# Kernel tuning notes

Hardware: AMD Instinct MI355X
Metric: run time of the kernel (lower is better)

## Reference

```python
import jax, jax.numpy as jnp
import numpy as np

B, F, C, H, W = 4, 16, 768, 16, 16   # video: b f c h w
L, M = 64, 16                        # audio: b c l m
NH = 12                              # num_heads
WS_V = 4                             # local_window (video window size, frames)
GROUPS = 32                          # GroupNorm32
EPS = 1e-5


def group_norm(x, scale, bias):
    # x: [b, c, t]; normalize over (channels-within-group, t)
    b, c, t = x.shape
    xg = x.reshape(b, GROUPS, c // GROUPS, t)
    mu = xg.mean(axis=(2, 3), keepdims=True)
    var = xg.var(axis=(2, 3), keepdims=True)
    xg = (xg - mu) * jax.lax.rsqrt(var + EPS)
    return xg.reshape(b, c, t) * scale[None, :, None] + bias[None, :, None]


def setup_inputs() -> dict:
    key = jax.random.key(0)
    ks = jax.random.split(key, 8)
    s = 0.02
    return {
        "video": jax.random.normal(ks[0], (B, F, C, H, W), jnp.float32),
        "audio": jax.random.normal(ks[1], (B, C, L, M), jnp.float32),
        "vn_scale": jnp.ones((C,), jnp.float32),
        "vn_bias": jnp.zeros((C,), jnp.float32),
        "an_scale": jnp.ones((C,), jnp.float32),
        "an_bias": jnp.zeros((C,), jnp.float32),
        "vqkv_w": jax.random.normal(ks[2], (3 * C, C), jnp.float32) * s,
        "vqkv_b": jnp.zeros((3 * C,), jnp.float32),
        "aqkv_w": jax.random.normal(ks[3], (3 * C, C), jnp.float32) * s,
        "aqkv_b": jnp.zeros((3 * C,), jnp.float32),
        "vproj_w": jax.random.normal(ks[4], (C, C), jnp.float32) * s,  # zero_module in orig; random for nontrivial baseline
        "vproj_b": jnp.zeros((C,), jnp.float32),
        "aproj_w": jax.random.normal(ks[5], (C, C), jnp.float32) * s,
        "aproj_b": jnp.zeros((C,), jnp.float32),
    }


def reference(video, audio, vn_scale, vn_bias, an_scale, an_bias,
              vqkv_w, vqkv_b, aqkv_w, aqkv_b,
              vproj_w, vproj_b, aproj_w, aproj_b):
    b, f, c, h, w = video.shape
    _, _, l, m = audio.shape
    ch = c // NH
    scale = ch ** -0.25
    ws_audio = WS_V * l // f
    nwin = f // WS_V
    wsv_tok = WS_V * h * w      # video tokens per window
    wsa_tok = ws_audio * m      # audio tokens per window

    vt = jnp.transpose(video, (0, 2, 1, 3, 4)).reshape(b, c, f * h * w)  # b c (f h w)
    at = audio.reshape(b, c, l * m)                                       # b c (l m)

    # 1x1 conv qkv after GroupNorm
    vqkv = jnp.einsum('oc,bct->bot', vqkv_w, group_norm(vt, vn_scale, vn_bias)) + vqkv_b[None, :, None]
    aqkv = jnp.einsum('oc,bct->bot', aqkv_w, group_norm(at, an_scale, an_bias)) + aqkv_b[None, :, None]
    q_v, k_v, v_v = jnp.split(vqkv, 3, axis=1)
    q_a, k_a, v_a = jnp.split(aqkv, 3, axis=1)

    # attention_index with window_shift = 0
    va_index = (jnp.arange(wsa_tok)[None, :] + (jnp.arange(nwin) * wsa_tok)[:, None]) % (l * m)
    av_index = (jnp.arange(wsv_tok)[None, :] + (jnp.arange(nwin) * wsv_tok)[:, None]) % (f * h * w)

    def heads(x):
        return x.reshape(b, NH, ch, -1)

    # video queries attend gathered audio windows
    qv = heads(q_v).reshape(b, NH, ch, nwin, wsv_tok)
    ka = jnp.take(heads(k_a), va_index, axis=-1)   # [b,NH,ch,nwin,wsa_tok]
    vav = jnp.take(heads(v_a), va_index, axis=-1)
    wts = jax.nn.softmax(jnp.einsum('bhcnt,bhcns->bhnts', qv * scale, ka * scale), axis=-1)
    v_out = jnp.einsum('bhnts,bhcns->bhcnt', wts, vav).reshape(b, c, f * h * w)

    # audio queries attend gathered video windows
    qa = heads(q_a).reshape(b, NH, ch, nwin, wsa_tok)
    kv = jnp.take(heads(k_v), av_index, axis=-1)   # [b,NH,ch,nwin,wsv_tok]
    vvv = jnp.take(heads(v_v), av_index, axis=-1)
    wts = jax.nn.softmax(jnp.einsum('bhcnt,bhcns->bhnts', qa * scale, kv * scale), axis=-1)
    a_out = jnp.einsum('bhnts,bhcns->bhcnt', wts, vvv).reshape(b, c, l * m)

    # zero-init 1x1x1 / 1x1 proj_out convs + residual
    vh = jnp.transpose(v_out.reshape(b, c, f, h, w), (0, 2, 1, 3, 4))  # b f c h w
    vh = jnp.einsum('oc,bfchw->bfohw', vproj_w, vh) + vproj_b[None, None, :, None, None]
    ah = jnp.einsum('oc,bclm->bolm', aproj_w, a_out.reshape(b, c, l, m)) + aproj_b[None, :, None, None]
    return video + vh, audio + ah
```

## Files before the change

### kernel.cpp

```cpp
#include <hip/hip_runtime.h>
#include <hip/hip_bf16.h>

typedef unsigned short ushort_t;
typedef __attribute__((ext_vector_type(8))) short short8;
typedef __attribute__((ext_vector_type(4))) float f32x4;

#define DI __device__ __forceinline__

DI float b2f(unsigned int u16) {
  union { unsigned int i; float f; } v;
  v.i = u16 << 16;
  return v.f;
}
DI ushort_t f2b(float f) {
  union { float f; unsigned int u; } v; v.f = f;
  unsigned int r = v.u + 0x7FFFu + ((v.u >> 16) & 1u);
  return (ushort_t)(r >> 16);
}

DI void gl_lds16(const ushort_t* g, ushort_t* l) {
  __builtin_amdgcn_global_load_lds(
      (const __attribute__((address_space(1))) unsigned int*)g,
      (__attribute__((address_space(3))) unsigned int*)l, 16, 0, 0);
}

__global__ __launch_bounds__(256) void fused_pre_kernel(
    const float* __restrict__ video, const float* __restrict__ audio,
    float* __restrict__ part,
    const float* __restrict__ w0, const float* __restrict__ w1,
    const float* __restrict__ w2, const float* __restrict__ w3,
    ushort_t* __restrict__ o0, ushort_t* __restrict__ o1,
    ushort_t* __restrict__ o2, ushort_t* __restrict__ o3) {
  const int bid = blockIdx.x;
  const int tid = threadIdx.x;
  __shared__ float red[8];
  if (bid < 2560) {
    float s = 0.f, ss = 0.f;
    if (bid < 2048) {
      int bg = bid >> 4, f = bid & 15;
      int b = bg >> 5, g = bg & 31;
      const float* base = video + ((size_t)((b * 16 + f) * 768 + g * 24)) * 256 + tid;
#pragma unroll
      for (int cl = 0; cl < 24; ++cl) {
        float v = base[cl * 256];
        s += v; ss += v * v;
      }
    } else {
      int a = bid - 2048;
      int bg = a >> 2, p = a & 3;
      int b = bg >> 5, g = bg & 31;
      const float* base = audio + ((size_t)(b * 768 + g * 24)) * 1024 + p * 256 + tid;
#pragma unroll
      for (int cl = 0; cl < 24; ++cl) {
        float v = base[cl * 1024];
        s += v; ss += v * v;
      }
    }
    for (int off = 32; off > 0; off >>= 1) { s += __shfl_down(s, off, 64); ss += __shfl_down(ss, off, 64); }
    int wv = tid >> 6, ln = tid & 63;
    if (ln == 0) { red[wv * 2] = s; red[wv * 2 + 1] = ss; }
    __syncthreads();
    if (tid == 0) {
      part[bid * 2] = red[0] + red[2] + red[4] + red[6];
      part[bid * 2 + 1] = red[1] + red[3] + red[5] + red[7];
    }
  } else {
    const int n1 = 2304 * 768, n3 = 768 * 768;
    const int total = 2 * n1 + 2 * n3;
    int wb = bid - 2560;
    for (int i = wb * 256 + tid; i < total; i += 1024 * 256) {
      if (i < n1) o0[i] = f2b(w0[i]);
      else if (i < 2 * n1) o1[i - n1] = f2b(w1[i - n1]);
      else if (i < 2 * n1 + n3) o2[i - 2 * n1] = f2b(w2[i - 2 * n1]);
      else o3[i - 2 * n1 - n3] = f2b(w3[i - 2 * n1 - n3]);
    }
  }
}

__global__ __launch_bounds__(256) void norm_fused_kernel(
    const float* __restrict__ video, const float* __restrict__ audio,
    const float* __restrict__ part,
    const float* __restrict__ vsc, const float* __restrict__ vbi,
    const float* __restrict__ asc, const float* __restrict__ abi,
    ushort_t* __restrict__ Xv, ushort_t* __restrict__ Xa) {
  __shared__ float T[32][257];
  __shared__ float shm[32], shr[32];
  const int bx = blockIdx.x;
  const int tid = threadIdx.x;
  if (bx < 1536) {
    const int bf = bx / 24, ct = bx % 24;
    const int b = bf >> 4, f = bf & 15;
    const int c0 = ct * 32;
    if (tid < 32) {
      int c = c0 + tid, g = c / 24;
      float s = 0.f, ss = 0.f;
#pragma unroll
      for (int i = 0; i < 16; ++i) {
        s += part[((b * 32 + g) * 16 + i) * 2];
        ss += part[((b * 32 + g) * 16 + i) * 2 + 1];
      }
      const float N = 24.f * 4096.f;
      float m = s / N;
      shm[tid] = m;
      shr[tid] = rsqrtf(ss / N - m * m + 1e-5f);
    }
    __syncthreads();
    for (int i = 0; i < 32; ++i) {
      int c = c0 + i;
      float v = video[((size_t)((b * 16 + f) * 768 + c)) * 256 + tid];
      T[i][tid] = (v - shm[i]) * shr[i] * vsc[c] + vbi[c];
    }
    __syncthreads();
    for (int i = 0; i < 32; ++i) {
      int id = i * 256 + tid;
      int c = id & 31, hw = id >> 5;
      Xv[((size_t)(b * 4096 + f * 256 + hw)) * 768 + c0 + c] = f2b(T[c][hw]);
    }
  } else {
    const int ax = bx - 1536;
    const int bt = ax / 24, ct = ax % 24;
    const int b = bt >> 2, t0 = (bt & 3) * 256;
    const int c0 = ct * 32;
    if (tid < 32) {
      int c = c0 + tid, g = c / 24;
      float s = 0.f, ss = 0.f;
#pragma unroll
      for (int i = 0; i < 4; ++i) {
        s += part[(2048 + (b * 32 + g) * 4 + i) * 2];
        ss += part[(2048 + (b * 32 + g) * 4 + i) * 2 + 1];
      }
      const float N = 24.f * 1024.f;
      float m = s / N;
      shm[tid] = m;
      shr[tid] = rsqrtf(ss / N - m * m + 1e-5f);
    }
    __syncthreads();
    for (int i = 0; i < 32; ++i) {
      int c = c0 + i;
      float v = audio[((size_t)(b * 768 + c)) * 1024 + t0 + tid];
      T[i][tid] = (v - shm[i]) * shr[i] * asc[c] + abi[c];
    }
    __syncthreads();
    for (int i = 0; i < 32; ++i) {
      int id = i * 256 + tid;
      int c = id & 31, tt = id >> 5;
      Xa[((size_t)(b * 1024 + t0 + tt)) * 768 + c0 + c] = f2b(T[c][tt]);
    }
  }
}

__global__ __launch_bounds__(256) void qkv_fused_kernel(
    const ushort_t* __restrict__ Xv, const ushort_t* __restrict__ Xa,
    const ushort_t* __restrict__ Wqv, const ushort_t* __restrict__ Wqa,
    const float* __restrict__ vqkv_b, const float* __restrict__ aqkv_b,
    ushort_t* __restrict__ Qv, ushort_t* __restrict__ Kv, ushort_t* __restrict__ Vv,
    ushort_t* __restrict__ Qa, ushort_t* __restrict__ Ka, ushort_t* __restrict__ Va) {
  __shared__ ushort_t sm[32768];
  const int bid = blockIdx.x;
  const int tid = threadIdx.x;
  const int lane = tid & 63, wave = tid >> 6;
  const int quad = lane >> 4, l16 = lane & 15;

  const bool isv = bid < 2304;
  const int lb = isv ? bid : bid - 2304;
  const int nwg = isv ? 2304 : 576;
  const ushort_t* A = isv ? Xv : Xa;
  const ushort_t* W = isv ? Wqv : Wqa;
  const float* bias = isv ? vqkv_b : aqkv_b;
  ushort_t* pQ = isv ? Qv : Qa;
  ushort_t* pK = isv ? Kv : Ka;
  ushort_t* pV = isv ? Vv : Va;
  const int M = isv ? 16384 : 4096;

  const int lid = (lb & 7) * (nwg >> 3) + (lb >> 3);
  const int n0 = (lid % 18) * 128, m0 = (lid / 18) * 128;
  const int wm = (wave & 1) * 64, wn = (wave >> 1) * 64;

  const int srow = wave * 32 + (lane >> 3);
  const int sq = ((lane & 7) ^ (lane >> 3)) * 8;
  const ushort_t* gA = A + (size_t)(m0 + srow) * 768 + sq;
  const ushort_t* gB = W + (size_t)(n0 + srow) * 768 + sq;

  f32x4 acc[4][4];
#pragma unroll
  for (int i = 0; i < 4; ++i)
#pragma unroll
    for (int j = 0; j < 4; ++j) acc[i][j] = (f32x4){0.f, 0.f, 0.f, 0.f};

  auto stage = [&](int kc, int cur) {
    ushort_t* lA = sm + cur * 8192 + wave * 2048;
    ushort_t* lB = sm + 16384 + cur * 8192 + wave * 2048;
#pragma unroll
    for (int i = 0; i < 4; ++i) {
      gl_lds16(gA + (size_t)i * 8 * 768 + kc, lA + i * 512);
      gl_lds16(gB + (size_t)i * 8 * 768 + kc, lB + i * 512);
    }
  };

  stage(0, 0);
  __syncthreads();
  int cur = 0;
  for (int t = 0; t < 12; ++t) {
    if (t < 11) stage((t + 1) * 64, cur ^ 1);
    const ushort_t* cA = sm + cur * 8192;
    const ushort_t* cB = sm + 16384 + cur * 8192;
#pragma unroll
    for (int ks = 0; ks < 2; ++ks) {
      short8 av[4], bv[4];
#pragma unroll
      for (int im = 0; im < 4; ++im) {
        int rr = wm + im * 16 + l16;
        av[im] = *reinterpret_cast<const short8*>(
            cA + rr * 64 + (((ks * 4 + quad) ^ (rr & 7)) * 8));
      }
#pragma unroll
      for (int in = 0; in < 4; ++in) {
        int rr = wn + in * 16 + l16;
        bv[in] = *reinterpret_cast<const short8*>(
            cB + rr * 64 + (((ks * 4 + quad) ^ (rr & 7)) * 8));
      }
#pragma unroll
      for (int im = 0; im < 4; ++im)
#pragma unroll
        for (int in = 0; in < 4; ++in)
          acc[im][in] = __builtin_amdgcn_mfma_f32_16x16x32_bf16(av[im], bv[in], acc[im][in], 0, 0, 0);
    }
    __syncthreads();
    cur ^= 1;
  }

  ushort_t* sC = sm;
  const int section = n0 / 768;
  const int obase = n0 - section * 768;
  if (section < 2) {
    const float qs = (section == 0) ? 0.125f : 1.0f;
#pragma unroll
    for (int in = 0; in < 4; ++in) {
      int ol = wn + in * 16 + l16;
      float bv_ = bias[n0 + ol];
#pragma unroll
      for (int im = 0; im < 4; ++im)
#pragma unroll
        for (int r = 0; r < 4; ++r) {
          int row = wm + im * 16 + quad * 4 + r;
          sC[row * 136 + ol] = f2b((acc[im][in][r] + bv_) * qs);
        }
    }
    __syncthreads();
    ushort_t* dst = (section == 0) ? pQ : pK;
#pragma unroll
    for (int i = 0; i < 8; ++i) {
      int cid = i * 256 + tid;
      int row = cid >> 4, ch = cid & 15;
      *reinterpret_cast<uint4*>(dst + (size_t)(m0 + row) * 768 + obase + ch * 8) =
          *reinterpret_cast<const uint4*>(sC + row * 136 + ch * 8);
    }
  } else {
#pragma unroll
    for (int in = 0; in < 4; ++in) {
      int ol = wn + in * 16 + l16;
      float bv_ = bias[n0 + ol];
#pragma unroll
      for (int im = 0; im < 4; ++im)
#pragma unroll
        for (int r = 0; r < 4; ++r) {
          int mr = wm + im * 16 + quad * 4 + r;
          sC[ol * 136 + mr] = f2b(acc[im][in][r] + bv_);
        }
    }
    __syncthreads();
#pragma unroll
    for (int i = 0; i < 8; ++i) {
      int cid = i * 256 + tid;
      int o = cid >> 4, ch = cid & 15;
      *reinterpret_cast<uint4*>(pV + (size_t)(obase + o) * M + m0 + ch * 8) =
          *reinterpret_cast<const uint4*>(sC + o * 136 + ch * 8);
    }
  }
}

__global__ __launch_bounds__(256) void proj_fused_kernel(
    const ushort_t* __restrict__ Ov, const ushort_t* __restrict__ Oa,
    const ushort_t* __restrict__ Wpv, const ushort_t* __restrict__ Wpa,
    const float* __restrict__ vproj_b, const float* __restrict__ aproj_b,
    float* __restrict__ out_v, const float* __restrict__ video,
    float* __restrict__ out_a, const float* __restrict__ audio) {
  __shared__ ushort_t sm[32768];
  const int bid = blockIdx.x;
  const int tid = threadIdx.x;
  const int lane = tid & 63, wave = tid >> 6;
  const int quad = lane >> 4, l16 = lane & 15;

  const bool isv = bid < 768;
  const int lb = isv ? bid : bid - 768;
  const int nwg = isv ? 768 : 192;
  const ushort_t* A = isv ? Ov : Oa;
  const ushort_t* W = isv ? Wpv : Wpa;
  const float* bias = isv ? vproj_b : aproj_b;
  float* outp = isv ? out_v : out_a;
  const float* resp = isv ? video : audio;

  const int lid = (lb & 7) * (nwg >> 3) + (lb >> 3);
  const int n0 = (lid % 6) * 128, m0 = (lid / 6) * 128;
  const int wm = (wave & 1) * 64, wn = (wave >> 1) * 64;

  const int srow = wave * 32 + (lane >> 3);
  const int sq = ((lane & 7) ^ (lane >> 3)) * 8;
  const ushort_t* gA = A + (size_t)(m0 + srow) * 768 + sq;
  const ushort_t* gB = W + (size_t)(n0 + srow) * 768 + sq;

  f32x4 acc[4][4];
#pragma unroll
  for (int i = 0; i < 4; ++i)
#pragma unroll
    for (int j = 0; j < 4; ++j) acc[i][j] = (f32x4){0.f, 0.f, 0.f, 0.f};

  auto stage = [&](int kc, int cur) {
    ushort_t* lA = sm + cur * 8192 + wave * 2048;
    ushort_t* lB = sm + 16384 + cur * 8192 + wave * 2048;
#pragma unroll
    for (int i = 0; i < 4; ++i) {
      gl_lds16(gA + (size_t)i * 8 * 768 + kc, lA + i * 512);
      gl_lds16(gB + (size_t)i * 8 * 768 + kc, lB + i * 512);
    }
  };

  stage(0, 0);
  __syncthreads();
  int cur = 0;
  for (int t = 0; t < 12; ++t) {
    if (t < 11) stage((t + 1) * 64, cur ^ 1);
    const ushort_t* cA = sm + cur * 8192;
    const ushort_t* cB = sm + 16384 + cur * 8192;
#pragma unroll
    for (int ks = 0; ks < 2; ++ks) {
      short8 av[4], bv[4];
#pragma unroll
      for (int im = 0; im < 4; ++im) {
        int rr = wm + im * 16 + l16;
        av[im] = *reinterpret_cast<const short8*>(
            cA + rr * 64 + (((ks * 4 + quad) ^ (rr & 7)) * 8));
      }
#pragma unroll
      for (int in = 0; in < 4; ++in) {
        int rr = wn + in * 16 + l16;
        bv[in] = *reinterpret_cast<const short8*>(
            cB + rr * 64 + (((ks * 4 + quad) ^ (rr & 7)) * 8));
      }
#pragma unroll
      for (int im = 0; im < 4; ++im)
#pragma unroll
        for (int in = 0; in < 4; ++in)
          acc[im][in] = __builtin_amdgcn_mfma_f32_16x16x32_bf16(av[im], bv[in], acc[im][in], 0, 0, 0);
    }
    __syncthreads();
    cur ^= 1;
  }

  ushort_t* sC = sm;
#pragma unroll
  for (int in = 0; in < 4; ++in) {
    int ol = wn + in * 16 + l16;
    float bv_ = bias[n0 + ol];
#pragma unroll
    for (int im = 0; im < 4; ++im)
#pragma unroll
      for (int r = 0; r < 4; ++r) {
        int mr = wm + im * 16 + quad * 4 + r;
        sC[ol * 136 + mr] = f2b(acc[im][in][r] + bv_);
      }
  }
  __syncthreads();
#pragma unroll
  for (int i = 0; i < 16; ++i) {
    int cid = i * 256 + tid;
    int o = cid >> 5, ch = cid & 31;
    uint2 pk = *reinterpret_cast<const uint2*>(sC + o * 136 + ch * 4);
    size_t gidx;
    if (isv) {
      int b = m0 >> 12, f = (m0 >> 8) & 15, hw0 = m0 & 255;
      gidx = ((size_t)((b * 16 + f) * 768 + n0 + o)) * 256 + hw0 + ch * 4;
    } else {
      int b = m0 >> 10, t0 = m0 & 1023;
      gidx = ((size_t)(b * 768 + n0 + o)) * 1024 + t0 + ch * 4;
    }
    float4 rv = *reinterpret_cast<const float4*>(resp + gidx);
    float4 ov;
    ov.x = rv.x + b2f(pk.x & 0xffff);
    ov.y = rv.y + b2f(pk.x >> 16);
    ov.z = rv.z + b2f(pk.y & 0xffff);
    ov.w = rv.w + b2f(pk.y >> 16);
    *reinterpret_cast<float4*>(outp + gidx) = ov;
  }
}

__global__ __launch_bounds__(256) void attn_fused_kernel(
    const ushort_t* __restrict__ Qv, const ushort_t* __restrict__ Ka,
    const ushort_t* __restrict__ Va, ushort_t* __restrict__ Ov,
    const ushort_t* __restrict__ Qa, const ushort_t* __restrict__ Kv,
    const ushort_t* __restrict__ Vv, ushort_t* __restrict__ Oa) {
  __shared__ ushort_t sm[37376];
  ushort_t* sQ = sm;
  ushort_t* sK = sm + 4096;
  ushort_t* sV0 = sm + 12288;
  ushort_t* sV1 = sm + 20480;
  ushort_t* sP = sm + 28672;
  const int tid = threadIdx.x;
  const int lane = tid & 63, wave = tid >> 6;
  const int quad = lane >> 4, l16 = lane & 15;
  const int bx = blockIdx.x;

  const bool isv = bx < 3072;
  const ushort_t* Qt = isv ? Qv : Qa;
  const ushort_t* Kt = isv ? Ka : Kv;
  const ushort_t* Vc = isv ? Va : Vv;
  ushort_t* Ot = isv ? Ov : Oa;
  const int lb = isv ? bx : bx - 3072;
  const int qlog = isv ? 4 : 2;
  const int NT = isv ? 2 : 8;
  const int QW = isv ? 1024 : 256;
  const int SW = isv ? 256 : 1024;
  const int TQb = isv ? 4096 : 1024;
  const int TSb = isv ? 1024 : 4096;
  const int Ms = isv ? 4096 : 16384;

  const int qt = lb & ((1 << qlog) - 1);
  const int win = (lb >> qlog) & 3;
  const int whb = lb >> (qlog + 2);
  const int h = whb % 12;
  const int batch = whb / 12;
  const int hc = h * 64;
  const int nq0 = batch * TQb + win * QW + qt * 64;
  const int ns_base = batch * TSb + win * SW;

  const int r8 = lane >> 3, c8 = lane & 7;
  const int s8 = (c8 ^ r8) * 8;
  const int r16 = lane >> 4, c16 = lane & 15;

  auto stage_k = [&](int ns0) {
#pragma unroll
    for (int i = 0; i < 4; ++i) {
      int row = wave * 32 + i * 8 + r8;
      gl_lds16(Kt + (size_t)(ns0 + row) * 768 + hc + s8, sK + (wave * 32 + i * 8) * 64);
    }
  };
  auto stage_v = [&](int ns0, ushort_t* sV) {
#pragma unroll
    for (int i = 0; i < 4; ++i) {
      int ch = wave * 16 + i * 4 + r16;
      int slot = c16 ^ (i * 4 + r16);
      gl_lds16(Vc + (size_t)(hc + ch) * Ms + ns0 + slot * 8, sV + (wave * 16 + i * 4) * 128);
    }
  };

#pragma unroll
  for (int i = 0; i < 2; ++i) {
    int row = wave * 16 + i * 8 + r8;
    gl_lds16(Qt + (size_t)(nq0 + row) * 768 + hc + s8, sQ + (wave * 16 + i * 8) * 64);
  }
  stage_k(ns_base);
  stage_v(ns_base, sV0);
  __syncthreads();

  short8 qf[2];
#pragma unroll
  for (int ks = 0; ks < 2; ++ks)
    qf[ks] = *reinterpret_cast<const short8*>(
        sQ + (wave * 16 + l16) * 64 + (((ks * 4 + quad) ^ (l16 & 7)) * 8));

  float mr[4], lr[4];
  f32x4 on[4];
#pragma unroll
  for (int r = 0; r < 4; ++r) { mr[r] = -1e30f; lr[r] = 0.f; }
#pragma unroll
  for (int nc = 0; nc < 4; ++nc) on[nc] = (f32x4){0.f, 0.f, 0.f, 0.f};

  for (int t = 0; t < NT; ++t) {
    if (t + 1 < NT) stage_v(ns_base + (t + 1) * 128, (t & 1) ? sV0 : sV1);
    f32x4 sf[8];
#pragma unroll
    for (int nt = 0; nt < 8; ++nt) sf[nt] = (f32x4){0.f, 0.f, 0.f, 0.f};
#pragma unroll
    for (int ks = 0; ks < 2; ++ks) {
#pragma unroll
      for (int nt = 0; nt < 8; ++nt) {
        short8 kf = *reinterpret_cast<const short8*>(
            sK + (nt * 16 + l16) * 64 + (((ks * 4 + quad) ^ (l16 & 7)) * 8));
        sf[nt] = __builtin_amdgcn_mfma_f32_16x16x32_bf16(qf[ks], kf, sf[nt], 0, 0, 0);
      }
    }
    __syncthreads();
    if (t + 1 < NT) stage_k(ns_base + (t + 1) * 128);
#pragma unroll
    for (int r = 0; r < 4; ++r) {
      float m_ = sf[0][r];
#pragma unroll
      for (int nt = 1; nt < 8; ++nt) m_ = fmaxf(m_, sf[nt][r]);
#pragma unroll
      for (int off = 1; off < 16; off <<= 1) m_ = fmaxf(m_, __shfl_xor(m_, off));
      float mnew = fmaxf(mr[r], m_);
      float al = __expf(mr[r] - mnew);
      float ls = 0.f;
      int prow = (wave * 16 + quad * 4 + r) * 136;
#pragma unroll
      for (int nt = 0; nt < 8; ++nt) {
        float p = __expf(sf[nt][r] - mnew);
        ls += p;
        sP[prow + nt * 16 + l16] = f2b(p);
      }
#pragma unroll
      for (int off = 1; off < 16; off <<= 1) ls += __shfl_xor(ls, off);
      lr[r] = lr[r] * al + ls;
      mr[r] = mnew;
#pragma unroll
      for (int nc = 0; nc < 4; ++nc) on[nc][r] *= al;
    }
    const ushort_t* sV = (t & 1) ? sV1 : sV0;
#pragma unroll
    for (int ks = 0; ks < 4; ++ks) {
      short8 pf = *reinterpret_cast<const short8*>(sP + (wave * 16 + l16) * 136 + ks * 32 + quad * 8);
#pragma unroll
      for (int nc = 0; nc < 4; ++nc) {
        short8 vf = *reinterpret_cast<const short8*>(
            sV + (nc * 16 + l16) * 128 + (((ks * 4 + quad) ^ l16) * 8));
        on[nc] = __builtin_amdgcn_mfma_f32_16x16x32_bf16(pf, vf, on[nc], 0, 0, 0);
      }
    }
    if (t + 1 < NT) __syncthreads();
  }
#pragma unroll
  for (int r = 0; r < 4; ++r) {
    float inv = 1.f / lr[r];
    int prow = (wave * 16 + quad * 4 + r) * 136;
#pragma unroll
    for (int nc = 0; nc < 4; ++nc)
      sP[prow + nc * 16 + l16] = f2b(on[nc][r] * inv);
  }
  __syncthreads();
#pragma unroll
  for (int i = 0; i < 2; ++i) {
    int c = i * 256 + tid;
    int row = c >> 3, cc = c & 7;
    *reinterpret_cast<uint4*>(Ot + (size_t)(nq0 + row) * 768 + hc + cc * 8) =
        *reinterpret_cast<const uint4*>(sP + row * 136 + cc * 8);
  }
}

extern "C" void kernel_launch(void* const* d_in, const int* in_sizes, int n_in,
                              void* d_out, int out_size, void* d_ws, size_t ws_size,
                              hipStream_t stream) {
  (void)in_sizes; (void)n_in; (void)out_size; (void)ws_size;
  const float* video = (const float*)d_in[0];
  const float* audio = (const float*)d_in[1];
  const float* vn_s = (const float*)d_in[2];
  const float* vn_b = (const float*)d_in[3];
  const float* an_s = (const float*)d_in[4];
  const float* an_b = (const float*)d_in[5];
  const float* vqkv_w = (const float*)d_in[6];
  const float* vqkv_b = (const float*)d_in[7];
  const float* aqkv_w = (const float*)d_in[8];
  const float* aqkv_b = (const float*)d_in[9];
  const float* vproj_w = (const float*)d_in[10];
  const float* vproj_b = (const float*)d_in[11];
  const float* aproj_w = (const float*)d_in[12];
  const float* aproj_b = (const float*)d_in[13];

  float* out_v = (float*)d_out;
  float* out_a = out_v + (size_t)4 * 16 * 768 * 16 * 16;

  char* ws = (char*)d_ws;
  size_t off = 0;
  auto carve = [&](size_t bytes) {
    char* p = ws + off;
    off += (bytes + 255) & ~(size_t)255;
    return p;
  };
  float* part = (float*)carve(2560 * 2 * 4);
  ushort_t* Xv = (ushort_t*)carve((size_t)16384 * 768 * 2);
  ushort_t* Xa = (ushort_t*)carve((size_t)4096 * 768 * 2);
  ushort_t* Wqv = (ushort_t*)carve((size_t)2304 * 768 * 2);
  ushort_t* Wqa = (ushort_t*)carve((size_t)2304 * 768 * 2);
  ushort_t* Wpv = (ushort_t*)carve((size_t)768 * 768 * 2);
  ushort_t* Wpa = (ushort_t*)carve((size_t)768 * 768 * 2);
  ushort_t* Qv = (ushort_t*)carve((size_t)16384 * 768 * 2);
  ushort_t* Kv = (ushort_t*)carve((size_t)16384 * 768 * 2);
  ushort_t* Vv = (ushort_t*)carve((size_t)16384 * 768 * 2);
  ushort_t* Qa = (ushort_t*)carve((size_t)4096 * 768 * 2);
  ushort_t* Ka = (ushort_t*)carve((size_t)4096 * 768 * 2);
  ushort_t* Va = (ushort_t*)carve((size_t)4096 * 768 * 2);
  ushort_t* Ov = Xv;
  ushort_t* Oa = Xa;

  fused_pre_kernel<<<3584, 256, 0, stream>>>(video, audio, part,
                                             vqkv_w, aqkv_w, vproj_w, aproj_w,
                                             Wqv, Wqa, Wpv, Wpa);
  norm_fused_kernel<<<1920, 256, 0, stream>>>(video, audio, part,
                                              vn_s, vn_b, an_s, an_b, Xv, Xa);
  qkv_fused_kernel<<<2880, 256, 0, stream>>>(Xv, Xa, Wqv, Wqa, vqkv_b, aqkv_b,
                                             Qv, Kv, Vv, Qa, Ka, Va);
  attn_fused_kernel<<<3840, 256, 0, stream>>>(Qv, Ka, Va, Ov, Qa, Kv, Vv, Oa);
  proj_fused_kernel<<<960, 256, 0, stream>>>(Ov, Oa, Wpv, Wpa, vproj_b, aproj_b,
                                             out_v, video, out_a, audio);
}
```

Measured before the change: 379.7 us.

## Load attention Q/K/V fragments directly from global memory and remap block order

Replaces the LDS-staged, double-buffered K/V pipeline with direct per-wave global loads of MFMA fragments, keeping only the P tile in shared memory and dropping most block barriers. It also remaps block indices so consecutive blocks interleave across the video and audio halves for better load balance and cache locality. The aim is to cut LDS traffic, barrier stalls and shared-memory footprint so more blocks fit per CU. The cost is that each of the four waves now reads the full K/V tiles from L2/global with strided 16-byte accesses and no explicit prefetch, so it relies on cache hits and occupancy to hide latency.

After: 705.3 us. 85.7% more time.

```diff
diff --git a/kernel.cpp b/kernel.cpp
--- a/kernel.cpp
+++ b/kernel.cpp
@@ -399,16 +399,13 @@
     const ushort_t* __restrict__ Va, ushort_t* __restrict__ Ov,
     const ushort_t* __restrict__ Qa, const ushort_t* __restrict__ Kv,
     const ushort_t* __restrict__ Vv, ushort_t* __restrict__ Oa) {
-  __shared__ ushort_t sm[37376];
-  ushort_t* sQ = sm;
-  ushort_t* sK = sm + 4096;
-  ushort_t* sV0 = sm + 12288;
-  ushort_t* sV1 = sm + 20480;
-  ushort_t* sP = sm + 28672;
+  __shared__ ushort_t sP[64 * 136];
   const int tid = threadIdx.x;
   const int lane = tid & 63, wave = tid >> 6;
   const int quad = lane >> 4, l16 = lane & 15;
-  const int bx = blockIdx.x;
+
+  const int bx0 = blockIdx.x;
+  const int bx = (bx0 & 7) * 480 + (bx0 >> 3);
 
   const bool isv = bx < 3072;
   const ushort_t* Qt = isv ? Qv : Qa;
@@ -433,40 +430,11 @@
   const int nq0 = batch * TQb + win * QW + qt * 64;
   const int ns_base = batch * TSb + win * SW;
 
-  const int r8 = lane >> 3, c8 = lane & 7;
-  const int s8 = (c8 ^ r8) * 8;
-  const int r16 = lane >> 4, c16 = lane & 15;
-
-  auto stage_k = [&](int ns0) {
-#pragma unroll
-    for (int i = 0; i < 4; ++i) {
-      int row = wave * 32 + i * 8 + r8;
-      gl_lds16(Kt + (size_t)(ns0 + row) * 768 + hc + s8, sK + (wave * 32 + i * 8) * 64);
-    }
-  };
-  auto stage_v = [&](int ns0, ushort_t* sV) {
-#pragma unroll
-    for (int i = 0; i < 4; ++i) {
-      int ch = wave * 16 + i * 4 + r16;
-      int slot = c16 ^ (i * 4 + r16);
-      gl_lds16(Vc + (size_t)(hc + ch) * Ms + ns0 + slot * 8, sV + (wave * 16 + i * 4) * 128);
-    }
-  };
-
-#pragma unroll
-  for (int i = 0; i < 2; ++i) {
-    int row = wave * 16 + i * 8 + r8;
-    gl_lds16(Qt + (size_t)(nq0 + row) * 768 + hc + s8, sQ + (wave * 16 + i * 8) * 64);
-  }
-  stage_k(ns_base);
-  stage_v(ns_base, sV0);
-  __syncthreads();
-
+  const ushort_t* qp = Qt + (size_t)(nq0 + wave * 16 + l16) * 768 + hc;
   short8 qf[2];
 #pragma unroll
   for (int ks = 0; ks < 2; ++ks)
-    qf[ks] = *reinterpret_cast<const short8*>(
-        sQ + (wave * 16 + l16) * 64 + (((ks * 4 + quad) ^ (l16 & 7)) * 8));
+    qf[ks] = *reinterpret_cast<const short8*>(qp + ks * 32 + quad * 8);
 
   float mr[4], lr[4];
   f32x4 on[4];
@@ -475,8 +443,12 @@
 #pragma unroll
   for (int nc = 0; nc < 4; ++nc) on[nc] = (f32x4){0.f, 0.f, 0.f, 0.f};
 
+  const ushort_t* kbase = Kt + (size_t)(ns_base + l16) * 768 + hc + quad * 8;
+  const ushort_t* vbase = Vc + (size_t)(hc + l16) * Ms + ns_base + quad * 8;
+  const int prow0 = (wave * 16 + quad * 4) * 136;
+
   for (int t = 0; t < NT; ++t) {
-    if (t + 1 < NT) stage_v(ns_base + (t + 1) * 128, (t & 1) ? sV0 : sV1);
+    const int toff = t * 128;
     f32x4 sf[8];
 #pragma unroll
     for (int nt = 0; nt < 8; ++nt) sf[nt] = (f32x4){0.f, 0.f, 0.f, 0.f};
@@ -485,12 +457,10 @@
 #pragma unroll
       for (int nt = 0; nt < 8; ++nt) {
         short8 kf = *reinterpret_cast<const short8*>(
-            sK + (nt * 16 + l16) * 64 + (((ks * 4 + quad) ^ (l16 & 7)) * 8));
+            kbase + (size_t)(toff + nt * 16) * 768 + ks * 32);
         sf[nt] = __builtin_amdgcn_mfma_f32_16x16x32_bf16(qf[ks], kf, sf[nt], 0, 0, 0);
       }
     }
-    __syncthreads();
-    if (t + 1 < NT) stage_k(ns_base + (t + 1) * 128);
 #pragma unroll
     for (int r = 0; r < 4; ++r) {
       float m_ = sf[0][r];
@@ -501,7 +471,7 @@
       float mnew = fmaxf(mr[r], m_);
       float al = __expf(mr[r] - mnew);
       float ls = 0.f;
-      int prow = (wave * 16 + quad * 4 + r) * 136;
+      int prow = prow0 + r * 136;
 #pragma unroll
       for (int nt = 0; nt < 8; ++nt) {
         float p = __expf(sf[nt][r] - mnew);
@@ -515,23 +485,21 @@
 #pragma unroll
       for (int nc = 0; nc < 4; ++nc) on[nc][r] *= al;
     }
-    const ushort_t* sV = (t & 1) ? sV1 : sV0;
 #pragma unroll
     for (int ks = 0; ks < 4; ++ks) {
       short8 pf = *reinterpret_cast<const short8*>(sP + (wave * 16 + l16) * 136 + ks * 32 + quad * 8);
 #pragma unroll
       for (int nc = 0; nc < 4; ++nc) {
         short8 vf = *reinterpret_cast<const short8*>(
-            sV + (nc * 16 + l16) * 128 + (((ks * 4 + quad) ^ l16) * 8));
+            vbase + (size_t)(nc * 16) * Ms + toff + ks * 32);
         on[nc] = __builtin_amdgcn_mfma_f32_16x16x32_bf16(pf, vf, on[nc], 0, 0, 0);
       }
     }
-    if (t + 1 < NT) __syncthreads();
   }
 #pragma unroll
   for (int r = 0; r < 4; ++r) {
     float inv = 1.f / lr[r];
-    int prow = (wave * 16 + quad * 4 + r) * 136;
+    int prow = prow0 + r * 136;
 #pragma unroll
     for (int nc = 0; nc < 4; ++nc)
       sP[prow + nc * 16 + l16] = f2b(on[nc][r] * inv);
```

## Fold log2e into Q scale, use exp2, MFMA row sums, and swizzle attention blocks

Applied to the files above, without the earlier changes.

The Q projection scale now includes log2(e), so the attention softmax can use the hardware exp2 directly instead of __expf. The per-row sum of P is no longer computed with a shuffle reduction. It is instead accumulated by an extra MFMA against a vector of bf16 ones, which also makes the normaliser consistent with the bf16-rounded P. The bf16 rounding of P is simplified to round-half-up, and the attention block index is remapped across 8 groups, likely to spread work across XCDs or improve cache locality. The aim is fewer VALU, shuffle and transcendental instructions in the softmax inner loop, at the cost of one extra MFMA per k-step.

Result: slower. 459.2 us (+20.9%).

```diff
diff --git a/kernel.cpp b/kernel.cpp
--- a/kernel.cpp
+++ b/kernel.cpp
@@ -233,7 +233,7 @@
   const int section = n0 / 768;
   const int obase = n0 - section * 768;
   if (section < 2) {
-    const float qs = (section == 0) ? 0.125f : 1.0f;
+    const float qs = (section == 0) ? 0.125f * 1.44269504088896340736f : 1.0f;
 #pragma unroll
     for (int in = 0; in < 4; ++in) {
       int ol = wn + in * 16 + l16;
@@ -408,7 +408,9 @@
   const int tid = threadIdx.x;
   const int lane = tid & 63, wave = tid >> 6;
   const int quad = lane >> 4, l16 = lane & 15;
-  const int bx = blockIdx.x;
+
+  const int bx0 = blockIdx.x;
+  const int bx = (bx0 & 7) * 480 + (bx0 >> 3);
 
   const bool isv = bx < 3072;
   const ushort_t* Qt = isv ? Qv : Qa;
@@ -468,12 +470,16 @@
     qf[ks] = *reinterpret_cast<const short8*>(
         sQ + (wave * 16 + l16) * 64 + (((ks * 4 + quad) ^ (l16 & 7)) * 8));
 
-  float mr[4], lr[4];
-  f32x4 on[4];
-#pragma unroll
-  for (int r = 0; r < 4; ++r) { mr[r] = -1e30f; lr[r] = 0.f; }
+  const short8 vones = {0x3F80, 0x3F80, 0x3F80, 0x3F80, 0x3F80, 0x3F80, 0x3F80, 0x3F80};
+
+  float mr[4];
+  f32x4 on[4], onl;
+#pragma unroll
+  for (int r = 0; r < 4; ++r) mr[r] = -1e30f;
 #pragma unroll
   for (int nc = 0; nc < 4; ++nc) on[nc] = (f32x4){0.f, 0.f, 0.f, 0.f};
+  onl = (f32x4){0.f, 0.f, 0.f, 0.f};
+  const int prow0 = (wave * 16 + quad * 4) * 136;
 
   for (int t = 0; t < NT; ++t) {
     if (t + 1 < NT) stage_v(ns_base + (t + 1) * 128, (t & 1) ? sV0 : sV1);
@@ -493,27 +499,24 @@
     if (t + 1 < NT) stage_k(ns_base + (t + 1) * 128);
 #pragma unroll
     for (int r = 0; r < 4; ++r) {
-      float m_ = sf[0][r];
-#pragma unroll
-      for (int nt = 1; nt < 8; ++nt) m_ = fmaxf(m_, sf[nt][r]);
+      float m_ = fmaxf(fmaxf(sf[0][r], sf[1][r]), sf[2][r]);
+      m_ = fmaxf(fmaxf(m_, sf[3][r]), sf[4][r]);
+      m_ = fmaxf(fmaxf(m_, sf[5][r]), sf[6][r]);
+      m_ = fmaxf(m_, sf[7][r]);
 #pragma unroll
       for (int off = 1; off < 16; off <<= 1) m_ = fmaxf(m_, __shfl_xor(m_, off));
       float mnew = fmaxf(mr[r], m_);
-      float al = __expf(mr[r] - mnew);
-      float ls = 0.f;
-      int prow = (wave * 16 + quad * 4 + r) * 136;
+      float al = __builtin_amdgcn_exp2f(mr[r] - mnew);
+      mr[r] = mnew;
+      int prow = prow0 + r * 136;
 #pragma unroll
       for (int nt = 0; nt < 8; ++nt) {
-        float p = __expf(sf[nt][r] - mnew);
-        ls += p;
-        sP[prow + nt * 16 + l16] = f2b(p);
-      }
-#pragma unroll
-      for (int off = 1; off < 16; off <<= 1) ls += __shfl_xor(ls, off);
-      lr[r] = lr[r] * al + ls;
-      mr[r] = mnew;
+        float p = __builtin_amdgcn_exp2f(sf[nt][r] - mnew);
+        sP[prow + nt * 16 + l16] = (ushort_t)((__float_as_uint(p) + 0x8000u) >> 16);
+      }
 #pragma unroll
       for (int nc = 0; nc < 4; ++nc) on[nc][r] *= al;
+      onl[r] *= al;
     }
     const ushort_t* sV = (t & 1) ? sV1 : sV0;
 #pragma unroll
@@ -525,13 +528,14 @@
             sV + (nc * 16 + l16) * 128 + (((ks * 4 + quad) ^ l16) * 8));
         on[nc] = __builtin_amdgcn_mfma_f32_16x16x32_bf16(pf, vf, on[nc], 0, 0, 0);
       }
+      onl = __builtin_amdgcn_mfma_f32_16x16x32_bf16(pf, vones, onl, 0, 0, 0);
     }
     if (t + 1 < NT) __syncthreads();
   }
 #pragma unroll
   for (int r = 0; r < 4; ++r) {
-    float inv = 1.f / lr[r];
-    int prow = (wave * 16 + quad * 4 + r) * 136;
+    float inv = 1.f / onl[r];
+    int prow = prow0 + r * 136;
 #pragma unroll
     for (int nc = 0; nc < 4; ++nc)
       sP[prow + nc * 16 + l16] = f2b(on[nc][r] * inv);
```
